# Performance work log

Hardware: AMD Instinct MI355X
Metric: run time of the kernel (lower is better)

Reference implementation:

```python
import jax, jax.numpy as jnp
import numpy as np

D = 1024
H = 16
HD = D // H
S = 2048
B = 4
EPS = 1e-5


def gelu_tanh(x):
    c = jnp.sqrt(2.0 / jnp.pi).astype(x.dtype)
    return 0.5 * x * (1.0 + jnp.tanh(c * (x + 0.044715 * x ** 3)))


def layernorm(x, gamma, beta):
    mu = jnp.mean(x, axis=-1, keepdims=True)
    var = jnp.var(x, axis=-1, keepdims=True)
    return (x - mu) * jax.lax.rsqrt(var + EPS) * gamma + beta


def setup_inputs() -> dict:
    key = jax.random.key(0)
    ks = jax.random.split(key, 12)
    s = 0.02
    return {
        "x": jax.random.normal(ks[0], (B, S, D), jnp.float32),
        "Wq": jax.random.normal(ks[1], (D, D), jnp.float32) * s,
        "Wk": jax.random.normal(ks[2], (D, D), jnp.float32) * s,
        "Wv": jax.random.normal(ks[3], (D, D), jnp.float32) * s,
        "Wo": jax.random.normal(ks[4], (D, D), jnp.float32) * s,
        "bo": jnp.zeros((D,), jnp.float32),
        "W1": jax.random.normal(ks[5], (D, 4 * D), jnp.float32) * s,
        "b1": jnp.zeros((4 * D,), jnp.float32),
        "W2": jax.random.normal(ks[6], (4 * D, D), jnp.float32) * s,
        "b2": jnp.zeros((D,), jnp.float32),
        "g1": jnp.ones((D,), jnp.float32),
        "be1": jnp.zeros((D,), jnp.float32),
        "g2": jnp.ones((D,), jnp.float32),
        "be2": jnp.zeros((D,), jnp.float32),
    }


def reference(x, Wq, Wk, Wv, Wo, bo, W1, b1, W2, b2, g1, be1, g2, be2):
    b, n, d = x.shape
    # --- attention sub-block (pre-LN) ---
    h = layernorm(x, g1, be1)
    q = (h @ Wq).reshape(b, n, H, HD).transpose(0, 2, 1, 3)  # [b,H,n,hd]
    k = (h @ Wk).reshape(b, n, H, HD).transpose(0, 2, 1, 3)
    v = (h @ Wv).reshape(b, n, H, HD).transpose(0, 2, 1, 3)
    scores = jnp.einsum('bhqd,bhkd->bhqk', q, k) / jnp.sqrt(jnp.float32(HD))
    causal = jnp.tril(jnp.ones((n, n), dtype=bool))
    scores = jnp.where(causal, scores, -jnp.inf)
    w = jax.nn.softmax(scores, axis=-1)  # dropout rate 0 -> identity
    attn = jnp.einsum('bhqk,bhkd->bhqd', w, v)
    attn = attn.transpose(0, 2, 1, 3).reshape(b, n, d)
    x = x + (attn @ Wo + bo)
    # --- FFN sub-block (pre-LN) ---
    h = layernorm(x, g2, be2)
    h = gelu_tanh(h @ W1 + b1) @ W2 + b2
    return x + h
```

## Files before the change

kernel.cpp:

```cpp
#include <hip/hip_runtime.h>
#include <hip/hip_bf16.h>
#include <math.h>


typedef __attribute__((ext_vector_type(8))) short bf16x8;
typedef __attribute__((ext_vector_type(4))) float f32x4;

#define AS1 __attribute__((address_space(1)))
#define AS3 __attribute__((address_space(3)))

__device__ __forceinline__ void gl_lds16(const void* g, void* l) {
  __builtin_amdgcn_global_load_lds((const AS1 void*)g, (AS3 void*)l, 16, 0, 0);
}

__device__ __forceinline__ float gelu_f(float x) {
  const float c = 0.7978845608028654f;
  return 0.5f * x * (1.0f + tanhf(c * (x + 0.044715f * x * x * x)));
}

__device__ __forceinline__ float bf2f(short s) {
  unsigned u = ((unsigned)(unsigned short)s) << 16;
  return __builtin_bit_cast(float, u);
}
__device__ __forceinline__ short f2bf(float f) {
  __hip_bfloat16 h = __float2bfloat16(f);
  return __builtin_bit_cast(short, h);
}

__global__ void __launch_bounds__(256) tcvt_kernel(
    const float* __restrict__ W, __hip_bfloat16* __restrict__ WT, int K, int N) {
  __shared__ float t[32][33];
  const int n0 = blockIdx.x * 32, k0 = blockIdx.y * 32;
  const int tx = threadIdx.x, ty0 = threadIdx.y;
#pragma unroll
  for (int i = 0; i < 4; i++) {
    int ty = ty0 + i * 8;
    t[ty][tx] = W[(size_t)(k0 + ty) * N + n0 + tx];
  }
  __syncthreads();
#pragma unroll
  for (int i = 0; i < 4; i++) {
    int ty = ty0 + i * 8;
    WT[(size_t)(n0 + ty) * K + k0 + tx] = __float2bfloat16(t[tx][ty]);
  }
}

__global__ void __launch_bounds__(256) vtr_kernel(
    const __hip_bfloat16* __restrict__ qkv, __hip_bfloat16* __restrict__ vt) {
  __shared__ __hip_bfloat16 t[32][33];
  const int s0 = blockIdx.x * 32;
  const int hd0 = blockIdx.y * 32;
  const int bh = blockIdx.z;
  const int b = bh >> 4, h = bh & 15;
  const int tx = threadIdx.x, ty0 = threadIdx.y;
  const __hip_bfloat16* src =
      qkv + (size_t)(b * 2048 + s0) * 3072 + 2048 + h * 64 + hd0;
#pragma unroll
  for (int i = 0; i < 4; i++) {
    int ty = ty0 + i * 8;
    t[ty][tx] = src[(size_t)ty * 3072 + tx];
  }
  __syncthreads();
  __hip_bfloat16* dst = vt + ((size_t)bh * 64 + hd0) * 2048 + s0;
#pragma unroll
  for (int i = 0; i < 4; i++) {
    int ty = ty0 + i * 8;
    dst[(size_t)ty * 2048 + tx] = t[tx][ty];
  }
}

__global__ void __launch_bounds__(256) ln_kernel(
    const float* __restrict__ x, const float* __restrict__ gma,
    const float* __restrict__ bta, __hip_bfloat16* __restrict__ out) {
  const int row = blockIdx.x;
  const int tid = threadIdx.x;
  const float4 v = ((const float4*)(x + (size_t)row * 1024))[tid];
  float s = v.x + v.y + v.z + v.w;
  float s2 = v.x * v.x + v.y * v.y + v.z * v.z + v.w * v.w;
#pragma unroll
  for (int m = 32; m; m >>= 1) {
    s += __shfl_xor(s, m);
    s2 += __shfl_xor(s2, m);
  }
  __shared__ float red[8];
  const int w = tid >> 6, lane = tid & 63;
  if (lane == 0) { red[w] = s; red[4 + w] = s2; }
  __syncthreads();
  s = red[0] + red[1] + red[2] + red[3];
  s2 = red[4] + red[5] + red[6] + red[7];
  const float mu = s * (1.0f / 1024.0f);
  const float var = s2 * (1.0f / 1024.0f) - mu * mu;
  const float rs = rsqrtf(var + 1e-5f);
  const float4 gv = ((const float4*)gma)[tid];
  const float4 bv = ((const float4*)bta)[tid];
  __hip_bfloat16* orow = out + (size_t)row * 1024 + tid * 4;
  orow[0] = __float2bfloat16((v.x - mu) * rs * gv.x + bv.x);
  orow[1] = __float2bfloat16((v.y - mu) * rs * gv.y + bv.y);
  orow[2] = __float2bfloat16((v.z - mu) * rs * gv.z + bv.z);
  orow[3] = __float2bfloat16((v.w - mu) * rs * gv.w + bv.w);
}

template <int BM, int BN, int EPI>
__global__ void __launch_bounds__(512, 2) gemm8(
    const __hip_bfloat16* __restrict__ Ap, const __hip_bfloat16* __restrict__ Bp,
    void* __restrict__ outp, const float* __restrict__ bias,
    const float* __restrict__ resid, int N, int K) {
  constexpr int PM = BM / 2;
  constexpr int MR = PM / 16;
  constexpr int NPH = MR / 2;
  constexpr int HA = BM / 128;
  constexpr int ABYTES = BM * 128;
  constexpr int BUFB = ABYTES + BN * 128;
  __shared__ __attribute__((aligned(128))) char smem[2 * BUFB];

  const int tid = threadIdx.x;
  const int lane = tid & 63, w = tid >> 6;
  const int wr = w >> 2, wc = w & 3;
  const int cr = lane & 15, g = lane >> 4;

  const int gx = gridDim.x;
  const int nwg = gx * gridDim.y;
  const int orig = blockIdx.y * gx + blockIdx.x;
  const int f = (orig & 7) * (nwg >> 3) + (orig >> 3);
  const int sid = f >> 4, wit = f & 15;
  const int stm = gx >> 2;
  const int bm = (sid % stm) * 4 + (wit & 3);
  const int bn = (sid / stm) * 4 + (wit >> 2);
  const int bmr = bm * BM, bnr = bn * BN;
  const int nkt = K >> 6;

  const int srow8 = lane >> 3;
  const int ssl = ((lane & 7) ^ srow8) * 8;
  unsigned aofs[2][2], bofs[2][2];
#pragma unroll
  for (int h = 0; h < 2; h++)
#pragma unroll
    for (int c = 0; c < 2; c++) {
      const int ha = (h < HA) ? h : 0;
      aofs[h][c] =
          (unsigned)(((bmr + ha * 128 + (w + c * 8) * 8 + srow8) * K + ssl) * 2);
      bofs[h][c] =
          (unsigned)(((bnr + h * 128 + (w + c * 8) * 8 + srow8) * K + ssl) * 2);
    }

  const int rk = cr & 7;
  const char* aP[2][2];
  const char* bP[2][2];
#pragma unroll
  for (int bf = 0; bf < 2; bf++)
#pragma unroll
    for (int ks = 0; ks < 2; ks++) {
      aP[bf][ks] =
          smem + bf * BUFB + (wr * PM + cr) * 128 + ((ks * 4 + g) ^ rk) * 16;
      bP[bf][ks] = smem + bf * BUFB + ABYTES + (wc * 64 + cr) * 128 +
                   ((ks * 4 + g) ^ rk) * 16;
    }

#define STG_A(BUF, tt, h)                                                     \
  do {                                                                        \
    const unsigned col = (unsigned)(tt) * 128u;                               \
    gl_lds16((const char*)Ap + aofs[h][0] + col,                              \
             smem + (BUF) * BUFB + (h) * 16384 + w * 1024);                   \
    gl_lds16((const char*)Ap + aofs[h][1] + col,                              \
             smem + (BUF) * BUFB + (h) * 16384 + (w + 8) * 1024);             \
  } while (0)
#define STG_B(BUF, tt, h)                                                     \
  do {                                                                        \
    const unsigned col = (unsigned)(tt) * 128u;                               \
    gl_lds16((const char*)Bp + bofs[h][0] + col,                              \
             smem + (BUF) * BUFB + ABYTES + (h) * 16384 + w * 1024);          \
    gl_lds16((const char*)Bp + bofs[h][1] + col,                              \
             smem + (BUF) * BUFB + ABYTES + (h) * 16384 + (w + 8) * 1024);    \
  } while (0)

  f32x4 acc[MR][4];
#pragma unroll
  for (int i = 0; i < MR; i++)
#pragma unroll
    for (int j = 0; j < 4; j++) acc[i][j] = (f32x4){0.f, 0.f, 0.f, 0.f};
  bf16x8 bv[4][2];

#pragma unroll
  for (int h = 0; h < HA; h++) STG_A(0, 0, h);
  STG_B(0, 0, 0); STG_B(0, 0, 1);
  STG_B(1, 1, 0); STG_B(1, 1, 1);
  asm volatile("s_waitcnt vmcnt(4)" ::: "memory");
  __builtin_amdgcn_s_barrier();

#define TILE_BODY(BUF, t)                                                     \
  {                                                                           \
    const int tA = ((t) + 1 < nkt) ? (t) + 1 : (t) - 1;                       \
    const int tB = ((t) + 2 < nkt) ? (t) + 2 : (t);                           \
    _Pragma("unroll") for (int q = 0; q < NPH; q++) {                         \
      bf16x8 av[2][2];                                                        \
      _Pragma("unroll") for (int mm = 0; mm < 2; mm++)                        \
          _Pragma("unroll") for (int ks = 0; ks < 2; ks++) av[mm][ks] =       \
          *(const bf16x8*)(aP[BUF][ks] + (q * 2 + mm) * 2048);                \
      if (q == 0) {                                                           \
        _Pragma("unroll") for (int n = 0; n < 4; n++)                         \
            _Pragma("unroll") for (int ks = 0; ks < 2; ks++) bv[n][ks] =      \
            *(const bf16x8*)(bP[BUF][ks] + n * 2048);                         \
      }                                                                       \
      if constexpr (NPH == 4) {                                               \
        if (q == 0) { STG_A((BUF) ^ 1, tA, 0); }                              \
        else if (q == 1) { STG_A((BUF) ^ 1, tA, 1); }                         \
        else if (q == 2) { STG_B(BUF, tB, 0); }                               \
        else { STG_B(BUF, tB, 1); }                                           \
      } else {                                                                \
        if (q == 0) { STG_A((BUF) ^ 1, tA, 0); }                              \
        else { STG_B(BUF, tB, 0); STG_B(BUF, tB, 1); }                        \
      }                                                                       \
      __builtin_amdgcn_s_barrier();                                           \
      asm volatile("s_waitcnt lgkmcnt(0)" ::: "memory");                      \
      __builtin_amdgcn_s_setprio(1);                                          \
      _Pragma("unroll") for (int mm = 0; mm < 2; mm++)                        \
          _Pragma("unroll") for (int n = 0; n < 4; n++)                       \
              _Pragma("unroll") for (int ks = 0; ks < 2; ks++)                \
                  acc[q * 2 + mm][n] =                                        \
          __builtin_amdgcn_mfma_f32_16x16x32_bf16(av[mm][ks], bv[n][ks],      \
                                                  acc[q * 2 + mm][n], 0, 0, 0); \
      __builtin_amdgcn_s_setprio(0);                                          \
      if (q == NPH - 1)                                                       \
        asm volatile("s_waitcnt vmcnt(4)" ::: "memory");                      \
      __builtin_amdgcn_s_barrier();                                           \
    }                                                                         \
  }

  for (int t = 0; t < nkt; t += 2) {
    TILE_BODY(0, t)
    TILE_BODY(1, t + 1)
  }
  asm volatile("s_waitcnt vmcnt(0)" ::: "memory");

#pragma unroll
  for (int m = 0; m < MR; m++) {
#pragma unroll
    for (int rr = 0; rr < 4; rr++) {
      const int row = bmr + wr * PM + m * 16 + g * 4 + rr;
#pragma unroll
      for (int n = 0; n < 4; n++) {
        const int col = bnr + wc * 64 + n * 16 + cr;
        float v = acc[m][n][rr];
        if (EPI == 0) {
          ((__hip_bfloat16*)outp)[(size_t)row * N + col] = __float2bfloat16(v);
        } else if (EPI == 1) {
          v += bias[col] + resid[(size_t)row * N + col];
          ((float*)outp)[(size_t)row * N + col] = v;
        } else {
          v = gelu_f(v + bias[col]);
          ((__hip_bfloat16*)outp)[(size_t)row * N + col] = __float2bfloat16(v);
        }
      }
    }
  }
#undef STG_A
#undef STG_B
#undef TILE_BODY
}

__global__ void __launch_bounds__(256) attn_kernel(
    const __hip_bfloat16* __restrict__ qkv, const __hip_bfloat16* __restrict__ vt,
    __hip_bfloat16* __restrict__ o) {
  __shared__ __hip_bfloat16 sK[2][64 * 64];
  __shared__ __hip_bfloat16 sV[2][64 * 64];
  __shared__ __hip_bfloat16 pl[4][16][64];
  const int tid = threadIdx.x, lane = tid & 63, w = tid >> 6;
  const int bid = blockIdx.x;
  const int bh = (bid & 7) + 8 * ((bid >> 3) & 7);
  const int qt = 15 - (bid >> 6);
  const int b = bh >> 4, h = bh & 15;
  const int cr = lane & 15, g = lane >> 4;
  const int qr0 = qt * 128 + w * 32;
  const float NEG = -1e30f;
  const float SC2 = 0.18033688011112042f;
  const int sw = cr & 7;
  const int sg0 = (g ^ sw) * 8;
  const int sg1 = ((g ^ sw) ^ 4) * 8;
  const int pkey = (cr & 7) << 1;

  bf16x8 aq[2][2];
#pragma unroll
  for (int m = 0; m < 2; m++) {
    const __hip_bfloat16* qp =
        qkv + (size_t)(b * 2048 + qr0 + m * 16 + cr) * 3072 + h * 64 + g * 8;
    bf16x8 q0 = *(const bf16x8*)qp;
    bf16x8 q1 = *(const bf16x8*)(qp + 32);
#pragma unroll
    for (int j = 0; j < 8; j++) {
      aq[m][0][j] = f2bf(bf2f(q0[j]) * SC2);
      aq[m][1][j] = f2bf(bf2f(q1[j]) * SC2);
    }
  }
  const __hip_bfloat16* kbase = qkv + (size_t)(b * 2048) * 3072 + 1024 + h * 64;
  const __hip_bfloat16* vbase = vt + (size_t)bh * 64 * 2048;

  const int l8 = lane >> 3, c8 = lane & 7;
  const int c8s = (c8 ^ l8) * 8;
#define STAGE_TILE(bi, ktile)                                                   \
  {                                                                             \
    _Pragma("unroll") for (int i = 0; i < 2; i++) {                             \
      const int rb = (i * 4 + w) * 8 + l8;                                      \
      gl_lds16(kbase + (size_t)((ktile) * 64 + rb) * 3072 + c8s,                \
               &sK[bi][(i * 4 + w) * 512]);                                     \
      gl_lds16(vbase + (size_t)rb * 2048 + (ktile) * 64 + c8s,                  \
               &sV[bi][(i * 4 + w) * 512]);                                     \
    }                                                                           \
  }

  f32x4 oacc[2][4];
#pragma unroll
  for (int m = 0; m < 2; m++)
#pragma unroll
    for (int i = 0; i < 4; i++) oacc[m][i] = (f32x4){0.f, 0.f, 0.f, 0.f};
  float mrow[2] = {NEG, NEG};
  float lrow[2] = {0.f, 0.f};

  const int nkt = (qt + 1) * 2;
  STAGE_TILE(0, 0);
  asm volatile("s_waitcnt vmcnt(0)" ::: "memory");
  __syncthreads();
  int cur = 0;

  for (int kt = 0; kt < nkt; ++kt) {
    if (kt + 1 < nkt) STAGE_TILE(cur ^ 1, kt + 1);

    if (kt * 64 <= qr0 + 31) {
      f32x4 st[4][2];
      __builtin_amdgcn_s_setprio(1);
#pragma unroll
      for (int kf = 0; kf < 4; kf++) {
        const bf16x8 bk0 = *(const bf16x8*)&sK[cur][(kf * 16 + cr) * 64 + sg0];
        const bf16x8 bk1 = *(const bf16x8*)&sK[cur][(kf * 16 + cr) * 64 + sg1];
#pragma unroll
        for (int mq = 0; mq < 2; mq++) {
          f32x4 z = (f32x4){0.f, 0.f, 0.f, 0.f};
          z = __builtin_amdgcn_mfma_f32_16x16x32_bf16(bk0, aq[mq][0], z, 0, 0, 0);
          z = __builtin_amdgcn_mfma_f32_16x16x32_bf16(bk1, aq[mq][1], z, 0, 0, 0);
          st[kf][mq] = z;
        }
      }
      __builtin_amdgcn_s_setprio(0);
      if (kt * 64 + 63 > qr0) {
#pragma unroll
        for (int kf = 0; kf < 4; kf++)
#pragma unroll
          for (int mq = 0; mq < 2; mq++)
#pragma unroll
            for (int rr = 0; rr < 4; rr++) {
              const int kvcol = kt * 64 + kf * 16 + g * 4 + rr;
              const int qrow = qr0 + mq * 16 + cr;
              if (kvcol > qrow) st[kf][mq][rr] = NEG;
            }
      }
#pragma unroll
      for (int mq = 0; mq < 2; mq++) {
        float pmax = st[0][mq][0];
#pragma unroll
        for (int kf = 0; kf < 4; kf++)
#pragma unroll
          for (int rr = 0; rr < 4; rr++)
            pmax = fmaxf(pmax, st[kf][mq][rr]);
        pmax = fmaxf(pmax, __shfl_xor(pmax, 16));
        pmax = fmaxf(pmax, __shfl_xor(pmax, 32));
        if (__any(pmax > mrow[mq] + 8.0f)) {
          const float mn = fmaxf(mrow[mq], pmax);
          const float scl = exp2f(mrow[mq] - mn);
          mrow[mq] = mn;
          lrow[mq] *= scl;
          float s0 = __shfl(scl, g * 4 + 0);
          float s1 = __shfl(scl, g * 4 + 1);
          float s2 = __shfl(scl, g * 4 + 2);
          float s3 = __shfl(scl, g * 4 + 3);
#pragma unroll
          for (int nf = 0; nf < 4; nf++) {
            f32x4 t = oacc[mq][nf];
            t[0] *= s0; t[1] *= s1; t[2] *= s2; t[3] *= s3;
            oacc[mq][nf] = t;
          }
        }
        float rsum = 0.f;
#pragma unroll
        for (int kf = 0; kf < 4; kf++) {
          short4 pk;
#pragma unroll
          for (int rr = 0; rr < 4; rr++) {
            const float p = exp2f(st[kf][mq][rr] - mrow[mq]);
            rsum += p;
            ((short*)&pk)[rr] = f2bf(p);
          }
          const int slot4 = (kf * 4 + g) ^ pkey;
          *(short4*)&pl[w][cr][slot4 * 4] = pk;
        }
        rsum += __shfl_xor(rsum, 16);
        rsum += __shfl_xor(rsum, 32);
        lrow[mq] += rsum;
        const bf16x8 pa0 = *(const bf16x8*)&pl[w][cr][((2 * g) ^ pkey) * 4];
        const bf16x8 pa1 = *(const bf16x8*)&pl[w][cr][((2 * g + 8) ^ pkey) * 4];
        __builtin_amdgcn_s_setprio(1);
#pragma unroll
        for (int nf = 0; nf < 4; nf++) {
          const bf16x8 bv0 = *(const bf16x8*)&sV[cur][(nf * 16 + cr) * 64 + sg0];
          const bf16x8 bv1 = *(const bf16x8*)&sV[cur][(nf * 16 + cr) * 64 + sg1];
          oacc[mq][nf] = __builtin_amdgcn_mfma_f32_16x16x32_bf16(pa0, bv0, oacc[mq][nf], 0, 0, 0);
          oacc[mq][nf] = __builtin_amdgcn_mfma_f32_16x16x32_bf16(pa1, bv1, oacc[mq][nf], 0, 0, 0);
        }
        __builtin_amdgcn_s_setprio(0);
      }
    }

    if (kt + 1 < nkt) {
      asm volatile("s_waitcnt vmcnt(0)" ::: "memory");
      __syncthreads();
      cur ^= 1;
    }
  }

#pragma unroll
  for (int m = 0; m < 2; m++) {
    float il[4];
#pragma unroll
    for (int rr = 0; rr < 4; rr++)
      il[rr] = 1.0f / __shfl(lrow[m], g * 4 + rr);
#pragma unroll
    for (int nf = 0; nf < 4; nf++)
#pragma unroll
      for (int rr = 0; rr < 4; rr++) {
        const int row = qr0 + m * 16 + g * 4 + rr;
        o[(size_t)(b * 2048 + row) * 1024 + h * 64 + nf * 16 + cr] =
            __float2bfloat16(oacc[m][nf][rr] * il[rr]);
      }
  }
#undef STAGE_TILE
}

extern "C" void kernel_launch(void* const* d_in, const int* in_sizes, int n_in,
                              void* d_out, int out_size, void* d_ws, size_t ws_size,
                              hipStream_t stream) {
  const float* x   = (const float*)d_in[0];
  const float* Wq  = (const float*)d_in[1];
  const float* Wk  = (const float*)d_in[2];
  const float* Wv  = (const float*)d_in[3];
  const float* Wo  = (const float*)d_in[4];
  const float* bo  = (const float*)d_in[5];
  const float* W1  = (const float*)d_in[6];
  const float* b1  = (const float*)d_in[7];
  const float* W2  = (const float*)d_in[8];
  const float* b2  = (const float*)d_in[9];
  const float* g1  = (const float*)d_in[10];
  const float* be1 = (const float*)d_in[11];
  const float* g2  = (const float*)d_in[12];
  const float* be2 = (const float*)d_in[13];

  char* ws = (char*)d_ws;
  const size_t MB = 1024 * 1024;
  __hip_bfloat16* hA    = (__hip_bfloat16*)(ws + 0);
  __hip_bfloat16* attnO = (__hip_bfloat16*)(ws + 0);
  __hip_bfloat16* qkv   = (__hip_bfloat16*)(ws + 16 * MB);
  float*          x2    = (float*)(ws + 16 * MB);
  __hip_bfloat16* h2    = (__hip_bfloat16*)(ws + 48 * MB);
  __hip_bfloat16* vtg   = (__hip_bfloat16*)(ws + 64 * MB);
  __hip_bfloat16* act   = (__hip_bfloat16*)(ws + 64 * MB);
  __hip_bfloat16* WqkvT = (__hip_bfloat16*)(ws + 128 * MB);
  __hip_bfloat16* WoT   = (__hip_bfloat16*)(ws + 134 * MB);
  __hip_bfloat16* W1T   = (__hip_bfloat16*)(ws + 136 * MB);
  __hip_bfloat16* W2T   = (__hip_bfloat16*)(ws + 144 * MB);

  const dim3 tb(32, 8);
  tcvt_kernel<<<dim3(32, 32), tb, 0, stream>>>(Wq, WqkvT, 1024, 1024);
  tcvt_kernel<<<dim3(32, 32), tb, 0, stream>>>(Wk, WqkvT + 1024 * 1024, 1024, 1024);
  tcvt_kernel<<<dim3(32, 32), tb, 0, stream>>>(Wv, WqkvT + 2 * 1024 * 1024, 1024, 1024);
  tcvt_kernel<<<dim3(32, 32), tb, 0, stream>>>(Wo, WoT, 1024, 1024);
  tcvt_kernel<<<dim3(128, 32), tb, 0, stream>>>(W1, W1T, 1024, 4096);
  tcvt_kernel<<<dim3(32, 128), tb, 0, stream>>>(W2, W2T, 4096, 1024);

  ln_kernel<<<8192, 256, 0, stream>>>(x, g1, be1, hA);
  gemm8<128, 256, 0><<<dim3(64, 12), 512, 0, stream>>>(
      hA, WqkvT, qkv, nullptr, nullptr, 3072, 1024);
  vtr_kernel<<<dim3(64, 2, 64), tb, 0, stream>>>(qkv, vtg);
  attn_kernel<<<1024, 256, 0, stream>>>(qkv, vtg, attnO);
  gemm8<128, 256, 1><<<dim3(64, 4), 512, 0, stream>>>(
      attnO, WoT, x2, bo, x, 1024, 1024);
  ln_kernel<<<8192, 256, 0, stream>>>(x2, g2, be2, h2);
  gemm8<256, 256, 2><<<dim3(32, 16), 512, 0, stream>>>(
      h2, W1T, act, b1, nullptr, 4096, 1024);
  gemm8<128, 256, 1><<<dim3(64, 4), 512, 0, stream>>>(
      act, W2T, (float*)d_out, b2, x2, 1024, 4096);
  (void)in_sizes; (void)n_in; (void)out_size; (void)ws_size;
}
```

Measured before the change: 387.6 us.

## Fuse weight conversions, restructure gemm8 barriers, add 128x128 GEMM for FFN down-proj

The six weight transpose/convert launches are merged into one kernel that dispatches on block index, cutting launch overhead. The gemm8 main loop moves its vmcnt wait and barrier to the start of each tile and drops the per-phase trailing barrier, so there are fewer synchronisations per tile. The FFN down-projection (K=4096) now uses a new 128x128-tile, 256-thread GEMM with swizzled LDS and grouped block remapping, giving 512 blocks instead of 256 for better CU occupancy. That new kernel is single-buffered with two syncthreads per K step, so load latency is less hidden, and removing gemm8's trailing barrier may let LDS buffers be overwritten before every wave has read them.

```diff
diff --git a/kernel.cpp b/kernel.cpp
--- a/kernel.cpp
+++ b/kernel.cpp
@@ -27,10 +27,34 @@
   return __builtin_bit_cast(short, h);
 }
 
-__global__ void __launch_bounds__(256) tcvt_kernel(
-    const float* __restrict__ W, __hip_bfloat16* __restrict__ WT, int K, int N) {
+__global__ void __launch_bounds__(256) tcvt_all(
+    const float* __restrict__ Wq, const float* __restrict__ Wk,
+    const float* __restrict__ Wv, const float* __restrict__ Wo,
+    const float* __restrict__ W1, const float* __restrict__ W2,
+    __hip_bfloat16* __restrict__ WqkvT, __hip_bfloat16* __restrict__ WoT,
+    __hip_bfloat16* __restrict__ W1T, __hip_bfloat16* __restrict__ W2T) {
   __shared__ float t[32][33];
-  const int n0 = blockIdx.x * 32, k0 = blockIdx.y * 32;
+  const int bid = blockIdx.x;
+  const float* W;
+  __hip_bfloat16* WT;
+  int K, N, n0, k0;
+  if (bid < 4096) {
+    const int which = bid >> 10, r = bid & 1023;
+    K = 1024; N = 1024;
+    n0 = (r & 31) * 32; k0 = (r >> 5) * 32;
+    W = which == 0 ? Wq : which == 1 ? Wk : which == 2 ? Wv : Wo;
+    WT = which < 3 ? WqkvT + which * 1024 * 1024 : WoT;
+  } else if (bid < 8192) {
+    const int r = bid - 4096;
+    K = 1024; N = 4096;
+    n0 = (r & 127) * 32; k0 = (r >> 7) * 32;
+    W = W1; WT = W1T;
+  } else {
+    const int r = bid - 8192;
+    K = 4096; N = 1024;
+    n0 = (r & 31) * 32; k0 = (r >> 5) * 32;
+    W = W2; WT = W2T;
+  }
   const int tx = threadIdx.x, ty0 = threadIdx.y;
 #pragma unroll
   for (int i = 0; i < 4; i++) {
@@ -184,11 +208,11 @@
   for (int h = 0; h < HA; h++) STG_A(0, 0, h);
   STG_B(0, 0, 0); STG_B(0, 0, 1);
   STG_B(1, 1, 0); STG_B(1, 1, 1);
-  asm volatile("s_waitcnt vmcnt(4)" ::: "memory");
-  __builtin_amdgcn_s_barrier();
 
 #define TILE_BODY(BUF, t)                                                     \
   {                                                                           \
+    asm volatile("s_waitcnt vmcnt(4)" ::: "memory");                          \
+    __builtin_amdgcn_s_barrier();                                             \
     const int tA = ((t) + 1 < nkt) ? (t) + 1 : (t) - 1;                       \
     const int tB = ((t) + 2 < nkt) ? (t) + 2 : (t);                           \
     _Pragma("unroll") for (int q = 0; q < NPH; q++) {                         \
@@ -220,9 +244,6 @@
           __builtin_amdgcn_mfma_f32_16x16x32_bf16(av[mm][ks], bv[n][ks],      \
                                                   acc[q * 2 + mm][n], 0, 0, 0); \
       __builtin_amdgcn_s_setprio(0);                                          \
-      if (q == NPH - 1)                                                       \
-        asm volatile("s_waitcnt vmcnt(4)" ::: "memory");                      \
-      __builtin_amdgcn_s_barrier();                                           \
     }                                                                         \
   }
 
@@ -256,6 +277,91 @@
 #undef STG_A
 #undef STG_B
 #undef TILE_BODY
+}
+
+template <int EPI>
+__global__ void __launch_bounds__(256) gemm97(
+    const __hip_bfloat16* __restrict__ Ap, const __hip_bfloat16* __restrict__ Bp,
+    void* __restrict__ outp, const float* __restrict__ bias,
+    const float* __restrict__ resid, int N, int K) {
+  __shared__ __hip_bfloat16 sA[128 * 64];
+  __shared__ __hip_bfloat16 sB[128 * 64];
+  const int tid = threadIdx.x;
+  const int lane = tid & 63, w = tid >> 6;
+  const int wr = w >> 1, wc = w & 1;
+  const int cr = lane & 15, g = lane >> 4;
+
+  const int gx = gridDim.x;
+  const int nwg = gx * gridDim.y;
+  const int orig = blockIdx.y * gx + blockIdx.x;
+  const int f = (orig & 7) * (nwg >> 3) + (orig >> 3);
+  const int sid = f >> 4, wit = f & 15;
+  const int stm = gx >> 2;
+  const int bm = (sid % stm) * 4 + (wit & 3);
+  const int bn = (sid / stm) * 4 + (wit >> 2);
+  const int bmr = bm * 128, bnr = bn * 128;
+
+  const int l8 = lane >> 3;
+  const int ssl = ((lane & 7) ^ l8) * 8;
+  const int rk = cr & 7;
+
+  f32x4 acc[4][4];
+#pragma unroll
+  for (int i = 0; i < 4; i++)
+#pragma unroll
+    for (int j = 0; j < 4; j++) acc[i][j] = (f32x4){0.f, 0.f, 0.f, 0.f};
+
+  for (int k0 = 0; k0 < K; k0 += 64) {
+#pragma unroll
+    for (int i = 0; i < 4; i++) {
+      const int chunk = w * 4 + i;
+      const int row = chunk * 8 + l8;
+      gl_lds16(Ap + (size_t)(bmr + row) * K + k0 + ssl, sA + chunk * 512);
+      gl_lds16(Bp + (size_t)(bnr + row) * K + k0 + ssl, sB + chunk * 512);
+    }
+    __syncthreads();
+#pragma unroll
+    for (int ks = 0; ks < 2; ks++) {
+      bf16x8 a[4], b[4];
+#pragma unroll
+      for (int m = 0; m < 4; m++)
+        a[m] = *(const bf16x8*)(sA + (wr * 64 + m * 16 + cr) * 64 +
+                                ((ks * 4 + g) ^ rk) * 8);
+#pragma unroll
+      for (int n = 0; n < 4; n++)
+        b[n] = *(const bf16x8*)(sB + (wc * 64 + n * 16 + cr) * 64 +
+                                ((ks * 4 + g) ^ rk) * 8);
+#pragma unroll
+      for (int m = 0; m < 4; m++)
+#pragma unroll
+        for (int n = 0; n < 4; n++)
+          acc[m][n] =
+              __builtin_amdgcn_mfma_f32_16x16x32_bf16(a[m], b[n], acc[m][n], 0, 0, 0);
+    }
+    __syncthreads();
+  }
+
+#pragma unroll
+  for (int m = 0; m < 4; m++) {
+#pragma unroll
+    for (int rr = 0; rr < 4; rr++) {
+      const int row = bmr + wr * 64 + m * 16 + g * 4 + rr;
+#pragma unroll
+      for (int n = 0; n < 4; n++) {
+        const int col = bnr + wc * 64 + n * 16 + cr;
+        float v = acc[m][n][rr];
+        if (EPI == 0) {
+          ((__hip_bfloat16*)outp)[(size_t)row * N + col] = __float2bfloat16(v);
+        } else if (EPI == 1) {
+          v += bias[col] + resid[(size_t)row * N + col];
+          ((float*)outp)[(size_t)row * N + col] = v;
+        } else {
+          v = gelu_f(v + bias[col]);
+          ((__hip_bfloat16*)outp)[(size_t)row * N + col] = __float2bfloat16(v);
+        }
+      }
+    }
+  }
 }
 
 __global__ void __launch_bounds__(256) attn_kernel(
@@ -466,12 +572,8 @@
   __hip_bfloat16* W2T   = (__hip_bfloat16*)(ws + 144 * MB);
 
   const dim3 tb(32, 8);
-  tcvt_kernel<<<dim3(32, 32), tb, 0, stream>>>(Wq, WqkvT, 1024, 1024);
-  tcvt_kernel<<<dim3(32, 32), tb, 0, stream>>>(Wk, WqkvT + 1024 * 1024, 1024, 1024);
-  tcvt_kernel<<<dim3(32, 32), tb, 0, stream>>>(Wv, WqkvT + 2 * 1024 * 1024, 1024, 1024);
-  tcvt_kernel<<<dim3(32, 32), tb, 0, stream>>>(Wo, WoT, 1024, 1024);
-  tcvt_kernel<<<dim3(128, 32), tb, 0, stream>>>(W1, W1T, 1024, 4096);
-  tcvt_kernel<<<dim3(32, 128), tb, 0, stream>>>(W2, W2T, 4096, 1024);
+  tcvt_all<<<12288, tb, 0, stream>>>(Wq, Wk, Wv, Wo, W1, W2,
+                                     WqkvT, WoT, W1T, W2T);
 
   ln_kernel<<<8192, 256, 0, stream>>>(x, g1, be1, hA);
   gemm8<128, 256, 0><<<dim3(64, 12), 512, 0, stream>>>(
@@ -483,7 +585,7 @@
   ln_kernel<<<8192, 256, 0, stream>>>(x2, g2, be2, h2);
   gemm8<256, 256, 2><<<dim3(32, 16), 512, 0, stream>>>(
       h2, W1T, act, b1, nullptr, 4096, 1024);
-  gemm8<128, 256, 1><<<dim3(64, 4), 512, 0, stream>>>(
+  gemm97<1><<<dim3(64, 8), 256, 0, stream>>>(
       act, W2T, (float*)d_out, b2, x2, 1024, 4096);
   (void)in_sizes; (void)n_in; (void)out_size; (void)ws_size;
 }
```

After: 389.1 us. No clear change (+0.4%).
